# Optimization experiments

Measured on AMD Instinct MI355X. Metric: run time of the kernel, lower is better.

Reference implementation:

```python
import jax, jax.numpy as jnp
import numpy as np

FULL_SCALE = 256
THRESH = 15.0  # full_scale > 128 -> distance_threshold = 15


def bilinear_sample(img, x, y):
    # img: [C,Hi,Wi]; x,y: [...] in [-1,1]; align_corners=False, zero padding
    C, Hi, Wi = img.shape
    xg = ((x + 1.0) * Wi - 1.0) / 2.0
    yg = ((y + 1.0) * Hi - 1.0) / 2.0
    x0 = jnp.floor(xg).astype(jnp.int32); x1 = x0 + 1
    y0 = jnp.floor(yg).astype(jnp.int32); y1 = y0 + 1
    wx = xg - x0.astype(img.dtype); wy = yg - y0.astype(img.dtype)

    def gather(yi, xi):
        valid = (yi >= 0) & (yi < Hi) & (xi >= 0) & (xi < Wi)
        yc = jnp.clip(yi, 0, Hi - 1); xc = jnp.clip(xi, 0, Wi - 1)
        return img[:, yc, xc] * valid[None].astype(img.dtype)

    return (gather(y0, x0) * ((1 - wy) * (1 - wx))[None]
            + gather(y0, x1) * ((1 - wy) * wx)[None]
            + gather(y1, x0) * (wy * (1 - wx))[None]
            + gather(y1, x1) * (wy * wx)[None])  # [C, ...]


def setup_inputs() -> dict:
    key = jax.random.key(0)
    k1, k2 = jax.random.split(key)
    image_x = jax.random.normal(k1, (1, 64, 256, 256), dtype=jnp.float32)
    all_edges = jax.random.uniform(k2, (8, 32, 4), dtype=jnp.float32)
    return {"image_x": image_x, "all_edges": all_edges}


def reference(image_x, all_edges):
    H = W = FULL_SCALE
    rows = jnp.arange(H, dtype=image_x.dtype)
    cols = jnp.arange(W, dtype=image_x.dtype)
    Vs, Us = jnp.meshgrid(rows, cols, indexing='ij')
    UV = jnp.stack([Vs, Us], axis=-1)  # [H,W,2] as (row, col), matches torch UVs

    def per_group(edges):
        e = edges * FULL_SCALE
        e0, e1 = e[:, :2], e[:, 2:4]
        d = e1 - e0                                    # [E,2]
        L = jnp.sqrt((d * d).sum(-1))                  # [E]
        dn = d / jnp.maximum(L, 1e-4)[:, None]
        nrm = jnp.stack([dn[:, 1], -dn[:, 0]], -1)     # normals
        diff = UV[:, :, None, :] - e0                  # [H,W,E,2]
        nd = jnp.abs((diff * nrm).sum(-1))             # normal distances [H,W,E]
        dd = (diff * dn).sum(-1) / jnp.maximum(L, 1e-4)  # direction distances
        near0 = jnp.sqrt((diff * diff).sum(-1)) <= THRESH
        near1 = jnp.sqrt(((UV[:, :, None, :] - e1) ** 2).sum(-1)) <= THRESH
        m = ((nd <= THRESH) & (dd <= 1) & (dd >= 0)) | near0 | near1  # all_edge_mask
        edge_mask = m.any(-1)                          # [H,W]
        off = jnp.minimum(dd, 1.0 - dd)                # point offsets
        mf = m.astype(image_x.dtype)
        pinfo = (off * mf).sum(-1) / jnp.maximum(mf.sum(-1), 1e-4)  # [H,W]
        return edge_mask, pinfo

    edge_mask, pinfo = jax.vmap(per_group)(all_edges)  # [G,H,W], [G,H,W]

    # grid_sample at every grid point (dense/masked equivalent of nonzero+gather);
    # torch swaps (v,u)->(u,v) so x = col, y = row, normalized p/size*2-1
    gx = (Us / FULL_SCALE) * 2.0 - 1.0
    gy = (Vs / FULL_SCALE) * 2.0 - 1.0
    sampled = bilinear_sample(image_x[0], gx, gy)      # [C,H,W]
    sampled = jnp.moveaxis(sampled, 0, -1)             # [H,W,C]

    G = all_edges.shape[0]
    feats = jnp.concatenate(
        [jnp.broadcast_to(sampled, (G,) + sampled.shape), pinfo[..., None]], axis=-1)
    feats = feats * edge_mask[..., None].astype(feats.dtype)  # zero non-edge pixels
    return feats, edge_mask
```

## Files before the change

### kernel.cpp

```cpp
#include <hip/hip_runtime.h>

#define HH 256
#define WW 256
#define CC 64
#define NG 8
#define NE 32
#define PX 32
#define THRESH 15.0f

typedef float f32x4 __attribute__((ext_vector_type(4)));

#define FEATS_ELEMS ((size_t)NG * HH * WW * 65)

#define IMG_ELEMS (CC * 2 * 33)

__global__ __launch_bounds__(256, 6) void fused_sparse_encoder(
    const float* __restrict__ img,
    const float* __restrict__ edges,
    float* __restrict__ out)
{
#pragma clang fp contract(off)
    __shared__ float  s_buf[66 * 65];
    __shared__ float4 s_k1[NG * NE];
    __shared__ float2 s_k2[NG * NE];
    __shared__ float  s_k3[NG * NE];
    __shared__ float  s_mask[NG * PX];
    __shared__ float  s_pinfo[NG * PX];

    const int tid = threadIdx.x;
    const int u0  = blockIdx.x * PX;
    const int v   = blockIdx.y;

    {
        const float4 e4 = reinterpret_cast<const float4*>(edges)[tid];
        const float e0v = e4.x * 256.0f;
        const float e0u = e4.y * 256.0f;
        const float e1v = e4.z * 256.0f;
        const float e1u = e4.w * 256.0f;
        const float d0 = e1v - e0v;
        const float d1 = e1u - e0u;
        const float L  = __fsqrt_rn(d0 * d0 + d1 * d1);
        const float Lm = fmaxf(L, 1e-4f);
        s_k1[tid] = make_float4(e0v, e0u, __fdiv_rn(d0, Lm), __fdiv_rn(d1, Lm));
        s_k2[tid] = make_float2(e1v, e1u);
        s_k3[tid] = Lm;
    }
    __syncthreads();

    float cbuf[17];
    #pragma unroll
    for (int t = 0; t < 17; ++t) {
        const int i = tid + t * 256;
        float val = 0.0f;
        if (i < IMG_ELEMS) {
            const int c  = i / 66;
            const int r  = i - c * 66;
            const int yy = r / 33;
            const int x  = r - yy * 33;
            const int gy = v - 1 + yy;
            const int gx = u0 - 1 + x;
            if (gy >= 0 && gx >= 0) {
                val = img[((size_t)c * HH + gy) * WW + gx];
            }
        }
        cbuf[t] = val;
    }

    {
        const int px = tid & (PX - 1);
        const int g  = tid >> 5;
        const float U = (float)(u0 + px);
        const float V = (float)v;
        float sm = 0.0f, cnt = 0.0f;
        bool any = false;
        for (int e = 0; e < NE; ++e) {
            const int idx = g * NE + e;
            const float4 k1 = s_k1[idx];
            const float2 k2 = s_k2[idx];
            const float  Lm = s_k3[idx];
            const float diff0 = V - k1.x;
            const float diff1 = U - k1.y;
            const float ndv = diff0 * k1.w - diff1 * k1.z;
            const float ddn = diff0 * k1.z + diff1 * k1.w;
            const float dd  = __fdiv_rn(ddn, Lm);
            const float r0sq = diff0 * diff0 + diff1 * diff1;
            const float f0 = V - k2.x;
            const float f1 = U - k2.y;
            const float r1sq = f0 * f0 + f1 * f1;
            const bool m = ((fabsf(ndv) <= THRESH) && (dd <= 1.0f) && (dd >= 0.0f))
                           || (r0sq <= 225.0f) || (r1sq <= 225.0f);
            if (m) {
                any = true;
                sm += fminf(dd, 1.0f - dd);
                cnt += 1.0f;
            }
        }
        const float pf = __fdiv_rn(sm, fmaxf(cnt, 1e-4f));
        const float mv = any ? 1.0f : 0.0f;
        s_mask[g * PX + px]  = mv;
        s_pinfo[g * PX + px] = pf;
        out[FEATS_ELEMS + ((size_t)g * HH + v) * WW + (u0 + px)] = mv;
    }

    #pragma unroll
    for (int t = 0; t < 17; ++t) {
        const int i = tid + t * 256;
        if (i < IMG_ELEMS) {
            const int c  = i / 66;
            const int r  = i - c * 66;
            const int yy = r / 33;
            const int x  = r - yy * 33;
            s_buf[(yy * 33 + x) * 65 + c] = cbuf[t];
        }
    }
    __syncthreads();

    const int wv   = tid >> 6;
    const int lane = tid & 63;
    float sreg[8];
    #pragma unroll
    for (int i = 0; i < 8; ++i) {
        const int p = wv * 8 + i;
        sreg[i] = s_buf[(p) * 65 + lane] * 0.25f
                + s_buf[(p + 1) * 65 + lane] * 0.25f
                + s_buf[(33 + p) * 65 + lane] * 0.25f
                + s_buf[(34 + p) * 65 + lane] * 0.25f;
    }
    __syncthreads();

    #pragma unroll
    for (int i = 0; i < 8; ++i) {
        const int p = wv * 8 + i;
        s_buf[p * 65 + lane] = sreg[i];
    }
    __syncthreads();

    for (int g = 0; g < NG; ++g) {
        const float* msk = &s_mask[g * PX];
        const float* pin = &s_pinfo[g * PX];
        float* gout = out + (((size_t)g * HH + v) * WW + u0) * 65;
        #pragma unroll
        for (int k = 0; k < 3; ++k) {
            const int q = tid + k * 256;
            if (q < 520) {
                const int f  = q * 4;
                const int p0 = (int)((unsigned)f / 65u);
                const int b  = (p0 + 1) * 65 - f;
                const float4 tv = *reinterpret_cast<const float4*>(&s_buf[f]);
                const float m0  = msk[p0];
                const float m1  = msk[(b < 4) ? (p0 + 1) : p0];
                const float pi0 = pin[p0];
                f32x4 r;
                r.x = ((b == 1) ? pi0 : tv.x) * ((0 < b) ? m0 : m1);
                r.y = ((b == 2) ? pi0 : tv.y) * ((1 < b) ? m0 : m1);
                r.z = ((b == 3) ? pi0 : tv.z) * ((2 < b) ? m0 : m1);
                r.w = ((b == 4) ? pi0 : tv.w) * ((3 < b) ? m0 : m1);
                __builtin_nontemporal_store(r, reinterpret_cast<f32x4*>(&gout[f]));
            }
        }
    }
}

extern "C" void kernel_launch(void* const* d_in, const int* in_sizes, int n_in,
                              void* d_out, int out_size, void* d_ws, size_t ws_size,
                              hipStream_t stream) {
    const float* img   = (const float*)d_in[0];
    const float* edges = (const float*)d_in[1];
    float* out = (float*)d_out;
    dim3 grid(WW / PX, HH);
    fused_sparse_encoder<<<grid, 256, 0, stream>>>(img, edges, out);
}
```

Before: 40.39 us.

## Split fused encoder into sample/mask kernel and streaming output kernel via workspace

Splits the single fused kernel into two. The first computes the bilinear samples, the edge mask and the pinfo, and writes them to a workspace. The second reloads these per-row tiles and streams the 8-group, 65-channel output with nontemporal stores, which lets the store-heavy phase run at higher occupancy with less shared memory. This adds a workspace round trip of about 16MB plus a second launch. The original fused kernel is kept as a fallback for when the workspace is too small.

```diff
diff --git a/kernel.cpp b/kernel.cpp
--- a/kernel.cpp
+++ b/kernel.cpp
@@ -11,25 +11,31 @@
 typedef float f32x4 __attribute__((ext_vector_type(4)));
 
 #define FEATS_ELEMS ((size_t)NG * HH * WW * 65)
+#define S_ELEMS  ((size_t)HH * WW * CC)
+#define MP_ELEMS ((size_t)NG * HH * WW)
+#define WS_NEEDED ((S_ELEMS + 2 * MP_ELEMS) * sizeof(float) + 64)
 
 #define IMG_ELEMS (CC * 2 * 33)
 
-__global__ __launch_bounds__(256, 6) void fused_sparse_encoder(
+__global__ __launch_bounds__(256, 6) void k1_sample_mask(
     const float* __restrict__ img,
     const float* __restrict__ edges,
-    float* __restrict__ out)
+    float* __restrict__ out,
+    float* __restrict__ S,
+    float* __restrict__ wm,
+    float* __restrict__ wp)
 {
 #pragma clang fp contract(off)
-    __shared__ float  s_buf[66 * 65];
+    __shared__ __align__(16) float s_buf[66 * 65];
     __shared__ float4 s_k1[NG * NE];
     __shared__ float2 s_k2[NG * NE];
     __shared__ float  s_k3[NG * NE];
-    __shared__ float  s_mask[NG * PX];
-    __shared__ float  s_pinfo[NG * PX];
-
-    const int tid = threadIdx.x;
-    const int u0  = blockIdx.x * PX;
-    const int v   = blockIdx.y;
+
+    const int tid  = threadIdx.x;
+    const int wv   = tid >> 6;
+    const int lane = tid & 63;
+    const int u0   = blockIdx.x * PX;
+    const int v    = blockIdx.y;
 
     {
         const float4 e4 = reinterpret_cast<const float4*>(edges)[tid];
@@ -97,9 +103,10 @@
         }
         const float pf = __fdiv_rn(sm, fmaxf(cnt, 1e-4f));
         const float mv = any ? 1.0f : 0.0f;
-        s_mask[g * PX + px]  = mv;
-        s_pinfo[g * PX + px] = pf;
-        out[FEATS_ELEMS + ((size_t)g * HH + v) * WW + (u0 + px)] = mv;
+        const size_t o = ((size_t)g * HH + v) * WW + (u0 + px);
+        wm[o] = mv;
+        wp[o] = pf;
+        out[FEATS_ELEMS + o] = mv;
     }
 
     #pragma unroll
@@ -115,8 +122,190 @@
     }
     __syncthreads();
 
+    #pragma unroll
+    for (int i = 0; i < 8; ++i) {
+        const int p = wv * 8 + i;
+        const float s = s_buf[(p) * 65 + lane] * 0.25f
+                      + s_buf[(p + 1) * 65 + lane] * 0.25f
+                      + s_buf[(33 + p) * 65 + lane] * 0.25f
+                      + s_buf[(34 + p) * 65 + lane] * 0.25f;
+        S[((size_t)v * WW + u0 + p) * CC + lane] = s;
+    }
+}
+
+__global__ __launch_bounds__(256, 8) void k2_stream(
+    const float* __restrict__ S,
+    const float* __restrict__ wm,
+    const float* __restrict__ wp,
+    float* __restrict__ out)
+{
+    __shared__ __align__(16) float s_S[PX * CC + 8];
+    __shared__ __align__(16) float s_m[NG * PX];
+    __shared__ __align__(16) float s_p[NG * PX];
+
+    const int tid = threadIdx.x;
+    const int u0  = blockIdx.x * PX;
+    const int v   = blockIdx.y;
+
+    {
+        const f32x4* src = reinterpret_cast<const f32x4*>(&S[((size_t)v * WW + u0) * CC]);
+        f32x4* dst = reinterpret_cast<f32x4*>(s_S);
+        dst[tid]       = src[tid];
+        dst[tid + 256] = src[tid + 256];
+    }
+    if (tid < 64) {
+        const int g = tid >> 3, j = tid & 7;
+        *reinterpret_cast<f32x4*>(&s_m[g * PX + 4 * j]) =
+            *reinterpret_cast<const f32x4*>(&wm[((size_t)g * HH + v) * WW + u0 + 4 * j]);
+    } else if (tid < 128) {
+        const int t2 = tid - 64;
+        const int g = t2 >> 3, j = t2 & 7;
+        *reinterpret_cast<f32x4*>(&s_p[g * PX + 4 * j]) =
+            *reinterpret_cast<const f32x4*>(&wp[((size_t)g * HH + v) * WW + u0 + 4 * j]);
+    }
+    __syncthreads();
+
+    int  e_f[3], e_p0[3], e_b[3];
+    bool e_on[3];
+    float ev0[3], ev1[3], ev2[3], ev3[3];
+    #pragma unroll
+    for (int k = 0; k < 3; ++k) {
+        const int q = tid + k * 256;
+        e_on[k] = (q < 520);
+        const int f  = q * 4;
+        const int p0 = (int)((unsigned)f / 65u);
+        e_f[k] = f; e_p0[k] = p0; e_b[k] = (p0 + 1) * 65 - f;
+        const int s0 = f - p0;
+        if (e_on[k]) {
+            ev0[k] = s_S[s0];
+            ev1[k] = s_S[s0 + 1];
+            ev2[k] = s_S[s0 + 2];
+            ev3[k] = s_S[s0 + 3];
+        }
+    }
+
+    for (int g = 0; g < NG; ++g) {
+        float* gout = out + (((size_t)g * HH + v) * WW + u0) * 65;
+        const float* mg = &s_m[g * PX];
+        const float* pg = &s_p[g * PX];
+        #pragma unroll
+        for (int k = 0; k < 3; ++k) {
+            if (e_on[k]) {
+                const int f  = e_f[k];
+                const int p0 = e_p0[k];
+                const int b  = e_b[k];
+                const float v0 = ev0[k], v1 = ev1[k], v2 = ev2[k], v3 = ev3[k];
+                const float m0 = mg[p0];
+                const float m1 = mg[(b < 4) ? (p0 + 1) : p0];
+                const float pi = pg[p0];
+                f32x4 r;
+                r.x = ((b == 1) ? pi : v0) * ((0 < b) ? m0 : m1);
+                r.y = ((b == 2) ? pi : ((b == 1) ? v0 : v1)) * ((1 < b) ? m0 : m1);
+                r.z = ((b == 3) ? pi : ((b <= 2) ? v1 : v2)) * ((2 < b) ? m0 : m1);
+                r.w = ((b == 4) ? pi : ((b <= 3) ? v2 : v3)) * ((3 < b) ? m0 : m1);
+                __builtin_nontemporal_store(r, reinterpret_cast<f32x4*>(&gout[f]));
+            }
+        }
+    }
+}
+
+__global__ __launch_bounds__(256, 6) void fused_sparse_encoder(
+    const float* __restrict__ img,
+    const float* __restrict__ edges,
+    float* __restrict__ out)
+{
+#pragma clang fp contract(off)
+    __shared__ __align__(16) float s_buf[66 * 65];
+    __shared__ float4 s_k1[NG * NE];
+    __shared__ float2 s_k2[NG * NE];
+    __shared__ float  s_k3[NG * NE];
+    __shared__ float  s_m[NG * PX];
+    __shared__ float  s_p[NG * PX];
+
+    const int tid  = threadIdx.x;
     const int wv   = tid >> 6;
     const int lane = tid & 63;
+    const int u0   = blockIdx.x * PX;
+    const int v    = blockIdx.y;
+
+    {
+        const float4 e4 = reinterpret_cast<const float4*>(edges)[tid];
+        const float e0v = e4.x * 256.0f;
+        const float e0u = e4.y * 256.0f;
+        const float e1v = e4.z * 256.0f;
+        const float e1u = e4.w * 256.0f;
+        const float d0 = e1v - e0v;
+        const float d1 = e1u - e0u;
+        const float L  = __fsqrt_rn(d0 * d0 + d1 * d1);
+        const float Lm = fmaxf(L, 1e-4f);
+        s_k1[tid] = make_float4(e0v, e0u, __fdiv_rn(d0, Lm), __fdiv_rn(d1, Lm));
+        s_k2[tid] = make_float2(e1v, e1u);
+        s_k3[tid] = Lm;
+    }
+    __syncthreads();
+
+    float cbuf[17];
+    #pragma unroll
+    for (int t = 0; t < 17; ++t) {
+        const int i = tid + t * 256;
+        float val = 0.0f;
+        if (i < IMG_ELEMS) {
+            const int c  = i / 66;
+            const int r  = i - c * 66;
+            const int yy = r / 33;
+            const int x  = r - yy * 33;
+            const int gy = v - 1 + yy;
+            const int gx = u0 - 1 + x;
+            if (gy >= 0 && gx >= 0) val = img[((size_t)c * HH + gy) * WW + gx];
+        }
+        cbuf[t] = val;
+    }
+
+    {
+        const int px = tid & (PX - 1);
+        const int g  = tid >> 5;
+        const float U = (float)(u0 + px);
+        const float V = (float)v;
+        float sm = 0.0f, cnt = 0.0f;
+        bool any = false;
+        for (int e = 0; e < NE; ++e) {
+            const int idx = g * NE + e;
+            const float4 k1 = s_k1[idx];
+            const float2 k2 = s_k2[idx];
+            const float  Lm = s_k3[idx];
+            const float diff0 = V - k1.x;
+            const float diff1 = U - k1.y;
+            const float ndv = diff0 * k1.w - diff1 * k1.z;
+            const float ddn = diff0 * k1.z + diff1 * k1.w;
+            const float dd  = __fdiv_rn(ddn, Lm);
+            const float r0sq = diff0 * diff0 + diff1 * diff1;
+            const float f0 = V - k2.x;
+            const float f1 = U - k2.y;
+            const float r1sq = f0 * f0 + f1 * f1;
+            const bool m = ((fabsf(ndv) <= THRESH) && (dd <= 1.0f) && (dd >= 0.0f))
+                           || (r0sq <= 225.0f) || (r1sq <= 225.0f);
+            if (m) { any = true; sm += fminf(dd, 1.0f - dd); cnt += 1.0f; }
+        }
+        const float pf = __fdiv_rn(sm, fmaxf(cnt, 1e-4f));
+        const float mv = any ? 1.0f : 0.0f;
+        s_m[g * PX + px] = mv;
+        s_p[g * PX + px] = pf;
+        out[FEATS_ELEMS + ((size_t)g * HH + v) * WW + (u0 + px)] = mv;
+    }
+
+    #pragma unroll
+    for (int t = 0; t < 17; ++t) {
+        const int i = tid + t * 256;
+        if (i < IMG_ELEMS) {
+            const int c  = i / 66;
+            const int r  = i - c * 66;
+            const int yy = r / 33;
+            const int x  = r - yy * 33;
+            s_buf[(yy * 33 + x) * 65 + c] = cbuf[t];
+        }
+    }
+    __syncthreads();
+
     float sreg[8];
     #pragma unroll
     for (int i = 0; i < 8; ++i) {
@@ -127,17 +316,15 @@
                 + s_buf[(34 + p) * 65 + lane] * 0.25f;
     }
     __syncthreads();
-
     #pragma unroll
     for (int i = 0; i < 8; ++i) {
-        const int p = wv * 8 + i;
-        s_buf[p * 65 + lane] = sreg[i];
+        s_buf[(wv * 8 + i) * 65 + lane] = sreg[i];
     }
     __syncthreads();
 
     for (int g = 0; g < NG; ++g) {
-        const float* msk = &s_mask[g * PX];
-        const float* pin = &s_pinfo[g * PX];
+        const float* msk = &s_m[g * PX];
+        const float* pin = &s_p[g * PX];
         float* gout = out + (((size_t)g * HH + v) * WW + u0) * 65;
         #pragma unroll
         for (int k = 0; k < 3; ++k) {
@@ -147,14 +334,14 @@
                 const int p0 = (int)((unsigned)f / 65u);
                 const int b  = (p0 + 1) * 65 - f;
                 const float4 tv = *reinterpret_cast<const float4*>(&s_buf[f]);
-                const float m0  = msk[p0];
-                const float m1  = msk[(b < 4) ? (p0 + 1) : p0];
-                const float pi0 = pin[p0];
+                const float m0 = msk[p0];
+                const float m1 = msk[(b < 4) ? (p0 + 1) : p0];
+                const float pi = pin[p0];
                 f32x4 r;
-                r.x = ((b == 1) ? pi0 : tv.x) * ((0 < b) ? m0 : m1);
-                r.y = ((b == 2) ? pi0 : tv.y) * ((1 < b) ? m0 : m1);
-                r.z = ((b == 3) ? pi0 : tv.z) * ((2 < b) ? m0 : m1);
-                r.w = ((b == 4) ? pi0 : tv.w) * ((3 < b) ? m0 : m1);
+                r.x = ((b == 1) ? pi : tv.x) * ((0 < b) ? m0 : m1);
+                r.y = ((b == 2) ? pi : tv.y) * ((1 < b) ? m0 : m1);
+                r.z = ((b == 3) ? pi : tv.z) * ((2 < b) ? m0 : m1);
+                r.w = ((b == 4) ? pi : tv.w) * ((3 < b) ? m0 : m1);
                 __builtin_nontemporal_store(r, reinterpret_cast<f32x4*>(&gout[f]));
             }
         }
@@ -167,6 +354,17 @@
     const float* img   = (const float*)d_in[0];
     const float* edges = (const float*)d_in[1];
     float* out = (float*)d_out;
-    dim3 grid(WW / PX, HH);
-    fused_sparse_encoder<<<grid, 256, 0, stream>>>(img, edges, out);
+
+    if (ws_size >= WS_NEEDED) {
+        float* S  = (float*)d_ws;
+        float* wm = S + S_ELEMS;
+        float* wp = wm + MP_ELEMS;
+        dim3 g1(WW / PX, HH);
+        k1_sample_mask<<<g1, 256, 0, stream>>>(img, edges, out, S, wm, wp);
+        dim3 g2(WW / PX, HH);
+        k2_stream<<<g2, 256, 0, stream>>>(S, wm, wp, out);
+    } else {
+        dim3 grid(WW / PX, HH);
+        fused_sparse_encoder<<<grid, 256, 0, stream>>>(img, edges, out);
+    }
 }
```

After: 59.02 us. +46.1%, slower.

## Use 64-stride shared tile, hoist output gathers out of group loop, inline edge prep

Applied to the files above, without the earlier changes.

Changes the shared image tile from a padded 65-float row to a dense 64-float row and rebuilds each 65-wide output vector from scalar shared reads with index remapping for the pinfo slot. The per-thread feature values are now loaded once before the 8-group store loop instead of once per group. Per-edge constants are no longer precomputed into shared memory; each thread recomputes sqrt and divisions inline for every edge, which adds ALU work to cut shared memory use. The occupancy hint goes from 6 to 7 blocks per CU.

```diff
diff --git a/kernel.cpp b/kernel.cpp
--- a/kernel.cpp
+++ b/kernel.cpp
@@ -14,37 +14,24 @@
 
 #define IMG_ELEMS (CC * 2 * 33)
 
-__global__ __launch_bounds__(256, 6) void fused_sparse_encoder(
+__global__ __launch_bounds__(256, 7) void fused_sparse_encoder(
     const float* __restrict__ img,
     const float* __restrict__ edges,
     float* __restrict__ out)
 {
 #pragma clang fp contract(off)
-    __shared__ float  s_buf[66 * 65];
-    __shared__ float4 s_k1[NG * NE];
-    __shared__ float2 s_k2[NG * NE];
-    __shared__ float  s_k3[NG * NE];
-    __shared__ float  s_mask[NG * PX];
-    __shared__ float  s_pinfo[NG * PX];
+    __shared__ __align__(16) float s_buf[66 * 64];
+    __shared__ __align__(16) float4 s_e[NG * NE];
+    __shared__ float s_m[NG * PX];
+    __shared__ float s_p[NG * PX];
 
-    const int tid = threadIdx.x;
-    const int u0  = blockIdx.x * PX;
-    const int v   = blockIdx.y;
+    const int tid  = threadIdx.x;
+    const int wv   = tid >> 6;
+    const int lane = tid & 63;
+    const int u0   = blockIdx.x * PX;
+    const int v    = blockIdx.y;
 
-    {
-        const float4 e4 = reinterpret_cast<const float4*>(edges)[tid];
-        const float e0v = e4.x * 256.0f;
-        const float e0u = e4.y * 256.0f;
-        const float e1v = e4.z * 256.0f;
-        const float e1u = e4.w * 256.0f;
-        const float d0 = e1v - e0v;
-        const float d1 = e1u - e0u;
-        const float L  = __fsqrt_rn(d0 * d0 + d1 * d1);
-        const float Lm = fmaxf(L, 1e-4f);
-        s_k1[tid] = make_float4(e0v, e0u, __fdiv_rn(d0, Lm), __fdiv_rn(d1, Lm));
-        s_k2[tid] = make_float2(e1v, e1u);
-        s_k3[tid] = Lm;
-    }
+    s_e[tid] = reinterpret_cast<const float4*>(edges)[tid];
     __syncthreads();
 
     float cbuf[17];
@@ -74,18 +61,25 @@
         float sm = 0.0f, cnt = 0.0f;
         bool any = false;
         for (int e = 0; e < NE; ++e) {
-            const int idx = g * NE + e;
-            const float4 k1 = s_k1[idx];
-            const float2 k2 = s_k2[idx];
-            const float  Lm = s_k3[idx];
-            const float diff0 = V - k1.x;
-            const float diff1 = U - k1.y;
-            const float ndv = diff0 * k1.w - diff1 * k1.z;
-            const float ddn = diff0 * k1.z + diff1 * k1.w;
+            const float4 e4 = s_e[g * NE + e];
+            const float e0v = e4.x * 256.0f;
+            const float e0u = e4.y * 256.0f;
+            const float e1v = e4.z * 256.0f;
+            const float e1u = e4.w * 256.0f;
+            const float d0 = e1v - e0v;
+            const float d1 = e1u - e0u;
+            const float L  = __fsqrt_rn(d0 * d0 + d1 * d1);
+            const float Lm = fmaxf(L, 1e-4f);
+            const float dn0 = __fdiv_rn(d0, Lm);
+            const float dn1 = __fdiv_rn(d1, Lm);
+            const float diff0 = V - e0v;
+            const float diff1 = U - e0u;
+            const float ndv = diff0 * dn1 - diff1 * dn0;
+            const float ddn = diff0 * dn0 + diff1 * dn1;
             const float dd  = __fdiv_rn(ddn, Lm);
             const float r0sq = diff0 * diff0 + diff1 * diff1;
-            const float f0 = V - k2.x;
-            const float f1 = U - k2.y;
+            const float f0 = V - e1v;
+            const float f1 = U - e1u;
             const float r1sq = f0 * f0 + f1 * f1;
             const bool m = ((fabsf(ndv) <= THRESH) && (dd <= 1.0f) && (dd >= 0.0f))
                            || (r0sq <= 225.0f) || (r1sq <= 225.0f);
@@ -97,8 +91,8 @@
         }
         const float pf = __fdiv_rn(sm, fmaxf(cnt, 1e-4f));
         const float mv = any ? 1.0f : 0.0f;
-        s_mask[g * PX + px]  = mv;
-        s_pinfo[g * PX + px] = pf;
+        s_m[g * PX + px] = mv;
+        s_p[g * PX + px] = pf;
         out[FEATS_ELEMS + ((size_t)g * HH + v) * WW + (u0 + px)] = mv;
     }
 
@@ -110,51 +104,66 @@
             const int r  = i - c * 66;
             const int yy = r / 33;
             const int x  = r - yy * 33;
-            s_buf[(yy * 33 + x) * 65 + c] = cbuf[t];
+            s_buf[(yy * 33 + x) * 64 + c] = cbuf[t];
         }
     }
     __syncthreads();
 
-    const int wv   = tid >> 6;
-    const int lane = tid & 63;
     float sreg[8];
     #pragma unroll
     for (int i = 0; i < 8; ++i) {
         const int p = wv * 8 + i;
-        sreg[i] = s_buf[(p) * 65 + lane] * 0.25f
-                + s_buf[(p + 1) * 65 + lane] * 0.25f
-                + s_buf[(33 + p) * 65 + lane] * 0.25f
-                + s_buf[(34 + p) * 65 + lane] * 0.25f;
+        sreg[i] = s_buf[(p) * 64 + lane] * 0.25f
+                + s_buf[(p + 1) * 64 + lane] * 0.25f
+                + s_buf[(33 + p) * 64 + lane] * 0.25f
+                + s_buf[(34 + p) * 64 + lane] * 0.25f;
     }
     __syncthreads();
 
     #pragma unroll
     for (int i = 0; i < 8; ++i) {
-        const int p = wv * 8 + i;
-        s_buf[p * 65 + lane] = sreg[i];
+        s_buf[(wv * 8 + i) * 64 + lane] = sreg[i];
     }
     __syncthreads();
 
+    int  e_p0[3], e_b[3], e_fq[3];
+    bool e_on[3];
+    float ev0[3], ev1[3], ev2[3], ev3[3];
+    #pragma unroll
+    for (int k = 0; k < 3; ++k) {
+        const int q = tid + k * 256;
+        e_on[k] = (q < 520);
+        const int f  = q * 4;
+        const int p0 = (int)((unsigned)f / 65u);
+        e_fq[k] = f; e_p0[k] = p0; e_b[k] = (p0 + 1) * 65 - f;
+        const int s0 = f - p0;
+        if (e_on[k]) {
+            ev0[k] = s_buf[s0];
+            ev1[k] = s_buf[s0 + 1];
+            ev2[k] = s_buf[s0 + 2];
+            ev3[k] = (s0 + 3 < 2048) ? s_buf[s0 + 3] : 0.0f;
+        }
+    }
+
     for (int g = 0; g < NG; ++g) {
-        const float* msk = &s_mask[g * PX];
-        const float* pin = &s_pinfo[g * PX];
         float* gout = out + (((size_t)g * HH + v) * WW + u0) * 65;
+        const float* mg = &s_m[g * PX];
+        const float* pg = &s_p[g * PX];
         #pragma unroll
         for (int k = 0; k < 3; ++k) {
-            const int q = tid + k * 256;
-            if (q < 520) {
-                const int f  = q * 4;
-                const int p0 = (int)((unsigned)f / 65u);
-                const int b  = (p0 + 1) * 65 - f;
-                const float4 tv = *reinterpret_cast<const float4*>(&s_buf[f]);
-                const float m0  = msk[p0];
-                const float m1  = msk[(b < 4) ? (p0 + 1) : p0];
-                const float pi0 = pin[p0];
+            if (e_on[k]) {
+                const int f  = e_fq[k];
+                const int p0 = e_p0[k];
+                const int b  = e_b[k];
+                const float v0 = ev0[k], v1 = ev1[k], v2 = ev2[k], v3 = ev3[k];
+                const float m0 = mg[p0];
+                const float m1 = mg[(b < 4) ? (p0 + 1) : p0];
+                const float pi = pg[p0];
                 f32x4 r;
-                r.x = ((b == 1) ? pi0 : tv.x) * ((0 < b) ? m0 : m1);
-                r.y = ((b == 2) ? pi0 : tv.y) * ((1 < b) ? m0 : m1);
-                r.z = ((b == 3) ? pi0 : tv.z) * ((2 < b) ? m0 : m1);
-                r.w = ((b == 4) ? pi0 : tv.w) * ((3 < b) ? m0 : m1);
+                r.x = ((b == 1) ? pi : v0) * ((0 < b) ? m0 : m1);
+                r.y = ((b == 2) ? pi : ((b == 1) ? v0 : v1)) * ((1 < b) ? m0 : m1);
+                r.z = ((b == 3) ? pi : ((b <= 2) ? v1 : v2)) * ((2 < b) ? m0 : m1);
+                r.w = ((b == 4) ? pi : ((b <= 3) ? v2 : v3)) * ((3 < b) ? m0 : m1);
                 __builtin_nontemporal_store(r, reinterpret_cast<f32x4*>(&gout[f]));
             }
         }
```

After: 52.00 us. +28.7%, slower.
